# Kernel tuning notes

Hardware: AMD Instinct MI355X
Metric: run time of the kernel (lower is better)

## Reference

```python
import jax, jax.numpy as jnp
import numpy as np

ENC_DIM, DEC_DIM, HID_DIM = 512, 1024, 128
B, T = 64, 2048


def setup_inputs() -> dict:
    key = jax.random.key(0)
    ks = jax.random.split(key, 8)
    encoder_outs = jax.random.normal(ks[0], (B, T, ENC_DIM), dtype=jnp.float32)
    decoder_state = jax.random.normal(ks[1], (B, DEC_DIM), dtype=jnp.float32)
    mask = jax.random.randint(ks[2], (B, T), 0, 2) == 1
    # parameters (torch nn.Linear: y = x @ W.T + b)
    sV = 1.0 / np.sqrt(ENC_DIM)
    sW = 1.0 / np.sqrt(DEC_DIM)
    sw = 1.0 / np.sqrt(HID_DIM)
    V_w = jax.random.uniform(ks[3], (HID_DIM, ENC_DIM), minval=-sV, maxval=sV)
    V_b = jax.random.uniform(ks[4], (HID_DIM,), minval=-sV, maxval=sV)
    W_w = jax.random.uniform(ks[5], (HID_DIM, DEC_DIM), minval=-sW, maxval=sW)
    w_w = jax.random.uniform(ks[6], (1, HID_DIM), minval=-sw, maxval=sw)
    w_b = jax.random.uniform(ks[7], (1,), minval=-sw, maxval=sw)
    return {"encoder_outs": encoder_outs, "decoder_state": decoder_state,
            "mask": mask, "V_w": V_w, "V_b": V_b, "W_w": W_w,
            "w_w": w_w, "w_b": w_b}


def reference(encoder_outs, decoder_state, mask, V_w, V_b, W_w, w_w, w_b):
    # [B,1,H] query projection + [B,T,H] key projection
    q = jnp.einsum('bd,hd->bh', decoder_state, W_w)[:, None, :]
    k = jnp.einsum('bte,he->bth', encoder_outs, V_w) + V_b
    # scores: [B,T]
    erg = jnp.einsum('bth,h->bt', jnp.tanh(q + k), w_w[0]) + w_b[0]
    erg = jnp.where(mask, -jnp.inf, erg)
    attention_weights = jax.nn.softmax(erg, axis=1)
    attention_context = jnp.einsum('bte,bt->be', encoder_outs, attention_weights)
    return (attention_context, attention_weights)
```

## Files before the change

### kernel.cpp

```cpp
#include <hip/hip_runtime.h>

#define Bn   64
#define Tn   2048
#define ENCD 512
#define DECD 1024
#define HIDD 128
#define TT   32
#define NCH  (Tn / TT)
#define CPG  8
#define NGR  (NCH / CPG)
#define LROW 520

typedef __attribute__((ext_vector_type(8))) short bf16x8;
typedef __attribute__((ext_vector_type(4))) float f32x4;

__device__ __forceinline__ unsigned short f2bf(float f) {
    union { float f; unsigned u; } v; v.f = f;
    unsigned r = v.u + 0x7FFFu + ((v.u >> 16) & 1u);
    return (unsigned short)(r >> 16);
}
__device__ __forceinline__ float bf2f(unsigned short s) {
    union { unsigned u; float f; } v; v.u = ((unsigned)s) << 16;
    return v.f;
}
__device__ __forceinline__ float tanh_fast(float x) {
    float xa = fminf(fmaxf(x, -10.f), 10.f);
    float e = __expf(2.f * xa);
    return (e - 1.f) / (e + 1.f);
}

__global__ __launch_bounds__(256) void prep(
    const float* __restrict__ dec, const float* __restrict__ Ww,
    const float* __restrict__ Vb,  const float* __restrict__ Vw,
    float* __restrict__ qb, unsigned short* __restrict__ Vbf)
{
    const int blk = blockIdx.x, tid = threadIdx.x;
    if (blk < 512) {
        const int b = blk >> 3, hg = blk & 7;
        const int h_local = tid >> 4, seg = tid & 15;
        const int h = hg * 16 + h_local;
        const float4* w = (const float4*)(Ww + (size_t)h * DECD);
        const float4* d = (const float4*)(dec + (size_t)b * DECD);
        float acc = 0.f;
        #pragma unroll
        for (int j = 0; j < 16; ++j) {
            int f4 = j * 16 + seg;
            float4 a = d[f4], bb = w[f4];
            acc += a.x * bb.x + a.y * bb.y + a.z * bb.z + a.w * bb.w;
        }
        acc += __shfl_xor(acc, 1);
        acc += __shfl_xor(acc, 2);
        acc += __shfl_xor(acc, 4);
        acc += __shfl_xor(acc, 8);
        if (seg == 0) qb[b * HIDD + h] = acc + Vb[h];
    } else {
        const int c = blk - 512;
        const float4* src = (const float4*)Vw;
        int f4 = c * 256 + tid;
        float4 v = src[f4];
        ushort4 u;
        u.x = f2bf(v.x); u.y = f2bf(v.y); u.z = f2bf(v.z); u.w = f2bf(v.w);
        *(ushort4*)&Vbf[f4 * 4] = u;
    }
}

__global__ __launch_bounds__(512, 4) void attn_main(
    const float* __restrict__ enc, const int* __restrict__ mask,
    const float* __restrict__ qb,  const unsigned short* __restrict__ Vbf,
    const float* __restrict__ ww,  const float* __restrict__ wb,
    float* __restrict__ pW, float* __restrict__ lC, float* __restrict__ ctxG)
{
    __shared__ unsigned short encS[2 * TT * LROW];
    __shared__ float wpart[8][TT];
    __shared__ float maskB[CPG * TT];

    const int cg = blockIdx.x, b = blockIdx.y;
    const int tid = threadIdx.x;
    const int wave = tid >> 6, lane = tid & 63;
    const int li = lane & 15, quad = lane >> 4;

    const int h = wave * 16 + li;
    const float qv = qb[b * HIDD + h];
    const float wv = ww[h];
    const unsigned short* vrow = Vbf + (size_t)h * ENCD;

    const float4* encBase =
        (const float4*)(enc + ((size_t)b * Tn + (size_t)cg * (CPG * TT)) * ENCD);

    if (tid < CPG * TT) {
        int mk = mask[b * Tn + cg * (CPG * TT) + tid];
        maskB[tid] = mk ? -INFINITY : wb[0];
    }

    float4 v[8];
    #pragma unroll
    for (int it = 0; it < 8; ++it) v[it] = encBase[it * 512 + tid];
    #pragma unroll
    for (int it = 0; it < 8; ++it) {
        int f4 = it * 512 + tid;
        int t = f4 >> 7, e2 = (f4 & 127) * 4;
        ushort4 u;
        u.x = f2bf(v[it].x); u.y = f2bf(v[it].y);
        u.z = f2bf(v[it].z); u.w = f2bf(v[it].w);
        *(ushort4*)&encS[t * LROW + e2] = u;
    }
    __syncthreads();

    float ctx = 0.f;

    for (int i = 0; i < CPG; ++i) {
        unsigned short* sb = encS + (i & 1) * (TT * LROW);
        const int chunk = cg * CPG + i;

        f32x4 acc[2];
        acc[0] = (f32x4){0.f, 0.f, 0.f, 0.f};
        acc[1] = (f32x4){0.f, 0.f, 0.f, 0.f};
        #pragma unroll 4
        for (int ks = 0; ks < 16; ++ks) {
            int k0 = ks * 32 + quad * 8;
            bf16x8 a0 = *(const bf16x8*)&sb[(0  + li) * LROW + k0];
            bf16x8 a1 = *(const bf16x8*)&sb[(16 + li) * LROW + k0];
            bf16x8 bb = *(const bf16x8*)(vrow + k0);
            acc[0] = __builtin_amdgcn_mfma_f32_16x16x32_bf16(a0, bb, acc[0], 0, 0, 0);
            acc[1] = __builtin_amdgcn_mfma_f32_16x16x32_bf16(a1, bb, acc[1], 0, 0, 0);
        }

        if (i + 1 < CPG) {
            #pragma unroll
            for (int it = 0; it < 8; ++it)
                v[it] = encBase[(i + 1) * (TT * ENCD / 4) + it * 512 + tid];
        }

        #pragma unroll
        for (int mt = 0; mt < 2; ++mt)
            #pragma unroll
            for (int r = 0; r < 4; ++r) {
                float s = tanh_fast(acc[mt][r] + qv) * wv;
                s += __shfl_xor(s, 1);
                s += __shfl_xor(s, 2);
                s += __shfl_xor(s, 4);
                s += __shfl_xor(s, 8);
                if (li == 0) wpart[wave][mt * 16 + quad * 4 + r] = s;
            }
        __syncthreads();

        {
            const int t = lane & 31;
            float es = maskB[i * TT + t];
            #pragma unroll
            for (int w = 0; w < 8; ++w) es += wpart[w][t];
            float p = __expf(es);

            if (wave == 0) {
                if (lane < TT)
                    pW[(size_t)b * Tn + chunk * TT + lane] = p;
                float ls = p;
                ls += __shfl_xor(ls, 1);
                ls += __shfl_xor(ls, 2);
                ls += __shfl_xor(ls, 4);
                ls += __shfl_xor(ls, 8);
                ls += __shfl_xor(ls, 16);
                if (lane == 0) lC[b * NCH + chunk] = ls;
            }

            #pragma unroll
            for (int t2 = 0; t2 < TT; ++t2)
                ctx += __shfl(p, t2) * bf2f(sb[t2 * LROW + tid]);
        }

        if (i + 1 < CPG) {
            unsigned short* nb = encS + ((i + 1) & 1) * (TT * LROW);
            #pragma unroll
            for (int it = 0; it < 8; ++it) {
                int f4 = it * 512 + tid;
                int t = f4 >> 7, e2 = (f4 & 127) * 4;
                ushort4 u;
                u.x = f2bf(v[it].x); u.y = f2bf(v[it].y);
                u.z = f2bf(v[it].z); u.w = f2bf(v[it].w);
                *(ushort4*)&nb[t * LROW + e2] = u;
            }
        }
        __syncthreads();
    }

    ctxG[((size_t)(b * NGR + cg)) * ENCD + tid] = ctx;
}

__global__ __launch_bounds__(512) void finalize(
    const float* __restrict__ lC, const float* __restrict__ pW,
    const float* __restrict__ ctxG, float* __restrict__ out)
{
    __shared__ float invLs;
    const int b = blockIdx.x, part = blockIdx.y, tid = threadIdx.x;
    const int wave = tid >> 6, lane = tid & 63;

    if (wave == 0) {
        float l = lC[b * NCH + lane];
        #pragma unroll
        for (int off = 32; off >= 1; off >>= 1)
            l += __shfl_xor(l, off);
        if (lane == 0) invLs = 1.f / l;
    }
    __syncthreads();
    const float invL = invLs;

    if (part == 0) {
        float c = 0.f;
        #pragma unroll
        for (int g = 0; g < NGR; ++g)
            c += ctxG[((size_t)(b * NGR + g)) * ENCD + tid];
        out[b * ENCD + tid] = c * invL;
    } else {
        float* outw = out + Bn * ENCD;
        #pragma unroll
        for (int i = 0; i < 4; ++i) {
            int t = i * 512 + tid;
            outw[(size_t)b * Tn + t] = pW[(size_t)b * Tn + t] * invL;
        }
    }
}

extern "C" void kernel_launch(void* const* d_in, const int* in_sizes, int n_in,
                              void* d_out, int out_size, void* d_ws, size_t ws_size,
                              hipStream_t stream)
{
    const float* enc  = (const float*)d_in[0];
    const float* dec  = (const float*)d_in[1];
    const int*   mask = (const int*)d_in[2];
    const float* Vw   = (const float*)d_in[3];
    const float* Vb   = (const float*)d_in[4];
    const float* Ww   = (const float*)d_in[5];
    const float* ww   = (const float*)d_in[6];
    const float* wb   = (const float*)d_in[7];
    float* out = (float*)d_out;
    float* ws  = (float*)d_ws;

    float*          qb   = ws;
    unsigned short* Vbf  = (unsigned short*)(ws + 8192);
    float*          pW   = ws + 40960;
    float*          lC   = ws + 172032;
    float*          ctxG = ws + 176128;

    hipLaunchKernelGGL(prep, dim3(576), dim3(256), 0, stream, dec, Ww, Vb, Vw, qb, Vbf);
    hipLaunchKernelGGL(attn_main, dim3(NGR, Bn), dim3(512), 0, stream,
                       enc, mask, qb, Vbf, ww, wb, pW, lC, ctxG);
    hipLaunchKernelGGL(finalize, dim3(Bn, 2), dim3(512), 0, stream, lC, pW, ctxG, out);
}
```

Measured before the change: 400.7 us.

## Assign one time chunk per block instead of persistent multi-chunk loop

Splits each batch row into 64 independent blocks, one per 32-step chunk, dropping the double-buffered in-block loop over 8 chunks. This raises the block count and occupancy to hide global-load latency, at the cost of losing explicit load/compute overlap. The finalize step now reduces 64 per-chunk context partials per batch instead of 8, adding extra workspace traffic.

```diff
diff --git a/kernel.cpp b/kernel.cpp
--- a/kernel.cpp
+++ b/kernel.cpp
@@ -7,8 +7,6 @@
 #define HIDD 128
 #define TT   32
 #define NCH  (Tn / TT)
-#define CPG  8
-#define NGR  (NCH / CPG)
 #define LROW 520
 
 typedef __attribute__((ext_vector_type(8))) short bf16x8;
@@ -64,131 +62,101 @@
     }
 }
 
-__global__ __launch_bounds__(512, 4) void attn_main(
+__global__ __launch_bounds__(512, 8) void attn_main(
     const float* __restrict__ enc, const int* __restrict__ mask,
     const float* __restrict__ qb,  const unsigned short* __restrict__ Vbf,
     const float* __restrict__ ww,  const float* __restrict__ wb,
-    float* __restrict__ pW, float* __restrict__ lC, float* __restrict__ ctxG)
-{
-    __shared__ unsigned short encS[2 * TT * LROW];
+    float* __restrict__ pW, float* __restrict__ lC, float* __restrict__ ctxP)
+{
+    __shared__ unsigned short encS[TT * LROW];
     __shared__ float wpart[8][TT];
-    __shared__ float maskB[CPG * TT];
-
-    const int cg = blockIdx.x, b = blockIdx.y;
+
+    const int chunk = blockIdx.x, b = blockIdx.y;
     const int tid = threadIdx.x;
     const int wave = tid >> 6, lane = tid & 63;
     const int li = lane & 15, quad = lane >> 4;
+    const int t0 = chunk * TT;
 
     const int h = wave * 16 + li;
     const float qv = qb[b * HIDD + h];
     const float wv = ww[h];
+    const int tm = lane & 31;
+    const float bias = (mask[b * Tn + t0 + tm] != 0) ? -INFINITY : wb[0];
+
+    const float4* encT4 = (const float4*)(enc + ((size_t)b * Tn + t0) * ENCD);
+    #pragma unroll
+    for (int half = 0; half < 2; ++half) {
+        float4 v4[4];
+        #pragma unroll
+        for (int it = 0; it < 4; ++it)
+            v4[it] = encT4[(half * 4 + it) * 512 + tid];
+        #pragma unroll
+        for (int it = 0; it < 4; ++it) {
+            int f4 = (half * 4 + it) * 512 + tid;
+            int t = f4 >> 7, e2 = (f4 & 127) * 4;
+            ushort4 u;
+            u.x = f2bf(v4[it].x); u.y = f2bf(v4[it].y);
+            u.z = f2bf(v4[it].z); u.w = f2bf(v4[it].w);
+            *(ushort4*)&encS[t * LROW + e2] = u;
+        }
+    }
+    __syncthreads();
+
+    f32x4 acc[2];
+    acc[0] = (f32x4){0.f, 0.f, 0.f, 0.f};
+    acc[1] = (f32x4){0.f, 0.f, 0.f, 0.f};
     const unsigned short* vrow = Vbf + (size_t)h * ENCD;
 
-    const float4* encBase =
-        (const float4*)(enc + ((size_t)b * Tn + (size_t)cg * (CPG * TT)) * ENCD);
-
-    if (tid < CPG * TT) {
-        int mk = mask[b * Tn + cg * (CPG * TT) + tid];
-        maskB[tid] = mk ? -INFINITY : wb[0];
-    }
-
-    float4 v[8];
-    #pragma unroll
-    for (int it = 0; it < 8; ++it) v[it] = encBase[it * 512 + tid];
-    #pragma unroll
-    for (int it = 0; it < 8; ++it) {
-        int f4 = it * 512 + tid;
-        int t = f4 >> 7, e2 = (f4 & 127) * 4;
-        ushort4 u;
-        u.x = f2bf(v[it].x); u.y = f2bf(v[it].y);
-        u.z = f2bf(v[it].z); u.w = f2bf(v[it].w);
-        *(ushort4*)&encS[t * LROW + e2] = u;
-    }
+    #pragma unroll 4
+    for (int ks = 0; ks < 16; ++ks) {
+        int k0 = ks * 32 + quad * 8;
+        bf16x8 a0 = *(const bf16x8*)&encS[(0  + li) * LROW + k0];
+        bf16x8 a1 = *(const bf16x8*)&encS[(16 + li) * LROW + k0];
+        bf16x8 bb = *(const bf16x8*)(vrow + k0);
+        acc[0] = __builtin_amdgcn_mfma_f32_16x16x32_bf16(a0, bb, acc[0], 0, 0, 0);
+        acc[1] = __builtin_amdgcn_mfma_f32_16x16x32_bf16(a1, bb, acc[1], 0, 0, 0);
+    }
+
+    #pragma unroll
+    for (int mt = 0; mt < 2; ++mt)
+        #pragma unroll
+        for (int r = 0; r < 4; ++r) {
+            float s = tanh_fast(acc[mt][r] + qv) * wv;
+            s += __shfl_xor(s, 1);
+            s += __shfl_xor(s, 2);
+            s += __shfl_xor(s, 4);
+            s += __shfl_xor(s, 8);
+            if (li == 0) wpart[wave][mt * 16 + quad * 4 + r] = s;
+        }
     __syncthreads();
 
-    float ctx = 0.f;
-
-    for (int i = 0; i < CPG; ++i) {
-        unsigned short* sb = encS + (i & 1) * (TT * LROW);
-        const int chunk = cg * CPG + i;
-
-        f32x4 acc[2];
-        acc[0] = (f32x4){0.f, 0.f, 0.f, 0.f};
-        acc[1] = (f32x4){0.f, 0.f, 0.f, 0.f};
-        #pragma unroll 4
-        for (int ks = 0; ks < 16; ++ks) {
-            int k0 = ks * 32 + quad * 8;
-            bf16x8 a0 = *(const bf16x8*)&sb[(0  + li) * LROW + k0];
-            bf16x8 a1 = *(const bf16x8*)&sb[(16 + li) * LROW + k0];
-            bf16x8 bb = *(const bf16x8*)(vrow + k0);
-            acc[0] = __builtin_amdgcn_mfma_f32_16x16x32_bf16(a0, bb, acc[0], 0, 0, 0);
-            acc[1] = __builtin_amdgcn_mfma_f32_16x16x32_bf16(a1, bb, acc[1], 0, 0, 0);
-        }
-
-        if (i + 1 < CPG) {
-            #pragma unroll
-            for (int it = 0; it < 8; ++it)
-                v[it] = encBase[(i + 1) * (TT * ENCD / 4) + it * 512 + tid];
-        }
-
-        #pragma unroll
-        for (int mt = 0; mt < 2; ++mt)
-            #pragma unroll
-            for (int r = 0; r < 4; ++r) {
-                float s = tanh_fast(acc[mt][r] + qv) * wv;
-                s += __shfl_xor(s, 1);
-                s += __shfl_xor(s, 2);
-                s += __shfl_xor(s, 4);
-                s += __shfl_xor(s, 8);
-                if (li == 0) wpart[wave][mt * 16 + quad * 4 + r] = s;
-            }
-        __syncthreads();
-
-        {
-            const int t = lane & 31;
-            float es = maskB[i * TT + t];
-            #pragma unroll
-            for (int w = 0; w < 8; ++w) es += wpart[w][t];
-            float p = __expf(es);
-
-            if (wave == 0) {
-                if (lane < TT)
-                    pW[(size_t)b * Tn + chunk * TT + lane] = p;
-                float ls = p;
-                ls += __shfl_xor(ls, 1);
-                ls += __shfl_xor(ls, 2);
-                ls += __shfl_xor(ls, 4);
-                ls += __shfl_xor(ls, 8);
-                ls += __shfl_xor(ls, 16);
-                if (lane == 0) lC[b * NCH + chunk] = ls;
-            }
-
-            #pragma unroll
-            for (int t2 = 0; t2 < TT; ++t2)
-                ctx += __shfl(p, t2) * bf2f(sb[t2 * LROW + tid]);
-        }
-
-        if (i + 1 < CPG) {
-            unsigned short* nb = encS + ((i + 1) & 1) * (TT * LROW);
-            #pragma unroll
-            for (int it = 0; it < 8; ++it) {
-                int f4 = it * 512 + tid;
-                int t = f4 >> 7, e2 = (f4 & 127) * 4;
-                ushort4 u;
-                u.x = f2bf(v[it].x); u.y = f2bf(v[it].y);
-                u.z = f2bf(v[it].z); u.w = f2bf(v[it].w);
-                *(ushort4*)&nb[t * LROW + e2] = u;
-            }
-        }
-        __syncthreads();
-    }
-
-    ctxG[((size_t)(b * NGR + cg)) * ENCD + tid] = ctx;
+    float es = bias;
+    #pragma unroll
+    for (int w = 0; w < 8; ++w) es += wpart[w][tm];
+    float p = __expf(es);
+
+    if (wave == 0) {
+        if (lane < TT)
+            pW[(size_t)b * Tn + t0 + lane] = p;
+        float ls = p;
+        ls += __shfl_xor(ls, 1);
+        ls += __shfl_xor(ls, 2);
+        ls += __shfl_xor(ls, 4);
+        ls += __shfl_xor(ls, 8);
+        ls += __shfl_xor(ls, 16);
+        if (lane == 0) lC[b * NCH + chunk] = ls;
+    }
+
+    float c = 0.f;
+    #pragma unroll
+    for (int t2 = 0; t2 < TT; ++t2)
+        c += __shfl(p, t2) * bf2f(encS[t2 * LROW + tid]);
+    ctxP[((size_t)(b * NCH + chunk)) * ENCD + tid] = c;
 }
 
 __global__ __launch_bounds__(512) void finalize(
     const float* __restrict__ lC, const float* __restrict__ pW,
-    const float* __restrict__ ctxG, float* __restrict__ out)
+    const float* __restrict__ ctxP, float* __restrict__ out)
 {
     __shared__ float invLs;
     const int b = blockIdx.x, part = blockIdx.y, tid = threadIdx.x;
@@ -206,9 +174,9 @@
 
     if (part == 0) {
         float c = 0.f;
-        #pragma unroll
-        for (int g = 0; g < NGR; ++g)
-            c += ctxG[((size_t)(b * NGR + g)) * ENCD + tid];
+        #pragma unroll 16
+        for (int cc = 0; cc < NCH; ++cc)
+            c += ctxP[((size_t)(b * NCH + cc)) * ENCD + tid];
         out[b * ENCD + tid] = c * invL;
     } else {
         float* outw = out + Bn * ENCD;
@@ -239,10 +207,10 @@
     unsigned short* Vbf  = (unsigned short*)(ws + 8192);
     float*          pW   = ws + 40960;
     float*          lC   = ws + 172032;
-    float*          ctxG = ws + 176128;
+    float*          ctxP = ws + 176128;
 
     hipLaunchKernelGGL(prep, dim3(576), dim3(256), 0, stream, dec, Ww, Vb, Vw, qb, Vbf);
-    hipLaunchKernelGGL(attn_main, dim3(NGR, Bn), dim3(512), 0, stream,
-                       enc, mask, qb, Vbf, ww, wb, pW, lC, ctxG);
-    hipLaunchKernelGGL(finalize, dim3(Bn, 2), dim3(512), 0, stream, lC, pW, ctxG, out);
-}
+    hipLaunchKernelGGL(attn_main, dim3(NCH, Bn), dim3(512), 0, stream,
+                       enc, mask, qb, Vbf, ww, wb, pW, lC, ctxP);
+    hipLaunchKernelGGL(finalize, dim3(Bn, 2), dim3(512), 0, stream, lC, pW, ctxP, out);
+}
```

Result: faster. 391.2 us (-2.4%).
